# Kernel tuning notes

Hardware: AMD Instinct MI355X
Metric: run time of the kernel (lower is better)

Reference implementation:

```python
import jax, jax.numpy as jnp
import numpy as np

TEMPERATURE = 0.07


def setup_inputs() -> dict:
    key = jax.random.key(0)
    k1, k2 = jax.random.split(key)
    B, D = 8192, 256
    embeddings = jax.random.normal(k1, (B, D), dtype=jnp.float32)
    ids = jax.random.randint(k2, (B,), 0, 1024, dtype=jnp.int64 if jax.config.jax_enable_x64 else jnp.int32)
    return {"embeddings": embeddings, "ids": ids}


def reference(embeddings, ids):
    B = embeddings.shape[0]
    # L2-normalize rows (F.normalize with p=2, dim=1)
    emb = embeddings / jnp.maximum(jnp.linalg.norm(embeddings, axis=1, keepdims=True), 1e-12)
    sim = (emb @ emb.T) / TEMPERATURE                      # [B, B]
    eye = jnp.eye(B, dtype=bool)
    sim = jnp.where(eye, -jnp.inf, sim)
    exp_sim = jnp.exp(sim)                                  # diag -> 0
    pos_mask = (ids[:, None] == ids[None, :]) & ~eye        # [B, B]
    pos_sum = jnp.sum(jnp.where(pos_mask, exp_sim, 0.0), axis=1)  # [B]
    all_sum = jnp.sum(exp_sim, axis=1)                      # [B]
    valid = pos_mask.any(axis=1)
    per_row = -jnp.log(pos_sum / all_sum)
    loss = jnp.sum(jnp.where(valid, per_row, 0.0))
    n_valid = jnp.sum(valid.astype(jnp.float32))
    return loss / jnp.maximum(n_valid, 1.0)
```

## Files before the change

### kernel.cpp

```cpp
#include <hip/hip_runtime.h>
#include <hip/hip_bf16.h>

#define B_SZ 8192
#define D_SZ 256
#define NTILES 2080
#define GRID_SIM 512
#define PRESCALE 4.539816004686735f

typedef __attribute__((ext_vector_type(4))) float f32x4;
typedef __attribute__((ext_vector_type(8))) short s16x8;

__global__ __launch_bounds__(256) void norm_kernel(const float* __restrict__ emb,
                                                   ushort* __restrict__ nbf,
                                                   float* __restrict__ sums) {
    sums[blockIdx.x * 64 + (threadIdx.x >> 2)] = 0.0f;

    const int wave = threadIdx.x >> 6, lane = threadIdx.x & 63;
    for (int g = blockIdx.x; g < B_SZ / 4; g += 256) {
        const int row = g * 4 + wave;
        const float4 v = ((const float4*)(emb + (size_t)row * D_SZ))[lane];
        float ss = v.x * v.x + v.y * v.y + v.z * v.z + v.w * v.w;
        #pragma unroll
        for (int m = 1; m < 64; m <<= 1) ss += __shfl_xor(ss, m, 64);
        float s = PRESCALE / fmaxf(sqrtf(ss), 1e-12f);
        __hip_bfloat16 b0 = __float2bfloat16(v.x * s);
        __hip_bfloat16 b1 = __float2bfloat16(v.y * s);
        __hip_bfloat16 b2 = __float2bfloat16(v.z * s);
        __hip_bfloat16 b3 = __float2bfloat16(v.w * s);
        ushort4 o;
        o.x = *(ushort*)&b0; o.y = *(ushort*)&b1; o.z = *(ushort*)&b2; o.w = *(ushort*)&b3;
        ((ushort4*)(nbf + (size_t)row * D_SZ))[lane] = o;
    }
}

__device__ __forceinline__ void decode_tile(int tb, int& i0, int& j0, bool& diag) {
    int bj = (int)((sqrtf(8.0f * tb + 1.0f) - 1.0f) * 0.5f);
    while ((bj + 1) * (bj + 2) / 2 <= tb) ++bj;
    while (bj * (bj + 1) / 2 > tb) --bj;
    const int bi = tb - bj * (bj + 1) / 2;
    i0 = bi * 128; j0 = bj * 128; diag = (bi == bj);
}

__device__ __forceinline__ void gload16(const ushort* g, ushort* l) {
    __builtin_amdgcn_global_load_lds(
        (const __attribute__((address_space(1))) unsigned int*)g,
        (__attribute__((address_space(3))) unsigned int*)l,
        16, 0, 0);
}

__device__ __forceinline__ void issue_stage(ushort* bA,
                                            const ushort* __restrict__ N,
                                            int i0, int j0, int k0,
                                            int wave, int r, int c8s) {
    ushort* bB = bA + 8192;
    const ushort* gA = N + (size_t)(i0 + wave * 32) * D_SZ + k0;
    const ushort* gB = N + (size_t)(j0 + wave * 32) * D_SZ + k0;
    #pragma unroll
    for (int q = 0; q < 4; ++q) {
        gload16(gA + (size_t)(q * 8 + r) * D_SZ + c8s, bA + (wave * 32 + q * 8) * 64);
        gload16(gB + (size_t)(q * 8 + r) * D_SZ + c8s, bB + (wave * 32 + q * 8) * 64);
    }
}

__global__ __launch_bounds__(256) void sim_kernel(const ushort* __restrict__ N,
                                                  const int* __restrict__ ids,
                                                  float* __restrict__ all_sum,
                                                  float* __restrict__ pos_sum) {
    __shared__ ushort smem[4 * 128 * 64];

    const int t    = threadIdx.x;
    const int wave = t >> 6, lane = t & 63;
    const int wy   = wave >> 1, wx = wave & 1;
    const int r    = lane >> 3;
    const int c8s  = ((lane & 7) ^ r) * 8;
    const int hi   = lane >> 4, myc = lane & 15;

    int tb = blockIdx.x;
    int i0, j0; bool diag;
    decode_tile(tb, i0, j0, diag);

    issue_stage(smem, N, i0, j0, 0, wave, r, c8s);

    while (true) {
        const int ntb = tb + GRID_SIM;
        const bool have_next = (ntb < NTILES);
        int ni0 = i0, nj0 = j0; bool ndiag = diag;
        if (have_next) decode_tile(ntb, ni0, nj0, ndiag);

        f32x4 acc[4][4];
        #pragma unroll
        for (int mi = 0; mi < 4; ++mi)
            #pragma unroll
            for (int ni = 0; ni < 4; ++ni)
                acc[mi][ni] = (f32x4){0.f, 0.f, 0.f, 0.f};

        #pragma unroll
        for (int kk = 0; kk < 4; ++kk) {
            ushort* bA = smem + (kk & 1) * 16384;
            ushort* bW = smem + ((kk + 1) & 1) * 16384;
            ushort* bB = bA + 8192;

            asm volatile("s_waitcnt vmcnt(0)" ::: "memory");
            __syncthreads();
            if (kk < 3)           issue_stage(bW, N, i0, j0, (kk + 1) * 64, wave, r, c8s);
            else if (have_next)   issue_stage(bW, N, ni0, nj0, 0, wave, r, c8s);

            #pragma unroll
            for (int ks = 0; ks < 2; ++ks) {
                const int C = ks * 4 + (lane >> 4);
                const int slot = (C ^ (lane & 7)) * 8;
                s16x8 af[4], bf[4];
                #pragma unroll
                for (int mi = 0; mi < 4; ++mi)
                    af[mi] = *(const s16x8*)&bA[(wy * 64 + mi * 16 + (lane & 15)) * 64 + slot];
                #pragma unroll
                for (int ni = 0; ni < 4; ++ni)
                    bf[ni] = *(const s16x8*)&bB[(wx * 64 + ni * 16 + (lane & 15)) * 64 + slot];
                #pragma unroll
                for (int mi = 0; mi < 4; ++mi)
                    #pragma unroll
                    for (int ni = 0; ni < 4; ++ni)
                        acc[mi][ni] = __builtin_amdgcn_mfma_f32_16x16x32_bf16(
                            af[mi], bf[ni], acc[mi][ni], 0, 0, 0);
            }
        }

        int idc[4];
        #pragma unroll
        for (int ni = 0; ni < 4; ++ni)
            idc[ni] = ids[j0 + wx * 64 + ni * 16 + myc];

        float cAll[4] = {0.f, 0.f, 0.f, 0.f};
        float cPos[4] = {0.f, 0.f, 0.f, 0.f};

        #pragma unroll
        for (int mi = 0; mi < 4; ++mi) {
            float rAll[4] = {0.f, 0.f, 0.f, 0.f};
            float rPos[4] = {0.f, 0.f, 0.f, 0.f};
            const int rbase = wy * 64 + mi * 16 + hi * 4;
            const int4 idr  = *(const int4*)&ids[i0 + rbase];
            #pragma unroll
            for (int ni = 0; ni < 4; ++ni) {
                const int cloc = wx * 64 + ni * 16 + myc;
                #pragma unroll
                for (int rg = 0; rg < 4; ++rg) {
                    float e = __builtin_amdgcn_exp2f(acc[mi][ni][rg]);
                    if (diag && (rbase + rg) == cloc) e = 0.0f;
                    rAll[rg] += e; cAll[ni] += e;
                    const int idrv = (rg == 0) ? idr.x : (rg == 1) ? idr.y
                                   : (rg == 2) ? idr.z : idr.w;
                    if (idrv == idc[ni]) { rPos[rg] += e; cPos[ni] += e; }
                }
            }
            #pragma unroll
            for (int rg = 0; rg < 4; ++rg) {
                #pragma unroll
                for (int m = 1; m < 16; m <<= 1) {
                    rAll[rg] += __shfl_xor(rAll[rg], m, 64);
                    rPos[rg] += __shfl_xor(rPos[rg], m, 64);
                }
            }
            if (myc == 0) {
                #pragma unroll
                for (int rg = 0; rg < 4; ++rg) {
                    atomicAdd(&all_sum[i0 + rbase + rg], rAll[rg]);
                    if (rPos[rg] != 0.0f) atomicAdd(&pos_sum[i0 + rbase + rg], rPos[rg]);
                }
            }
        }

        if (!diag) {
            #pragma unroll
            for (int ni = 0; ni < 4; ++ni) {
                cAll[ni] += __shfl_xor(cAll[ni], 16, 64);
                cAll[ni] += __shfl_xor(cAll[ni], 32, 64);
                cPos[ni] += __shfl_xor(cPos[ni], 16, 64);
                cPos[ni] += __shfl_xor(cPos[ni], 32, 64);
            }
            if (lane < 16) {
                #pragma unroll
                for (int ni = 0; ni < 4; ++ni) {
                    const int gc = j0 + wx * 64 + ni * 16 + lane;
                    atomicAdd(&all_sum[gc], cAll[ni]);
                    if (cPos[ni] != 0.0f) atomicAdd(&pos_sum[gc], cPos[ni]);
                }
            }
        }

        if (!have_next) break;
        tb = ntb; i0 = ni0; j0 = nj0; diag = ndiag;
    }
}

__global__ __launch_bounds__(256) void loss_kernel(const float* __restrict__ all_sum,
                                                   const float* __restrict__ pos_sum,
                                                   float* __restrict__ out) {
    float loss = 0.0f, cnt = 0.0f;
    for (int i = threadIdx.x; i < B_SZ; i += 256) {
        float p = pos_sum[i], a = all_sum[i];
        if (p > 0.0f) { loss += logf(a) - logf(p); cnt += 1.0f; }
    }
    #pragma unroll
    for (int m = 1; m < 64; m <<= 1) {
        loss += __shfl_xor(loss, m, 64);
        cnt  += __shfl_xor(cnt, m, 64);
    }
    __shared__ float sl[4], sc[4];
    int wave = threadIdx.x >> 6, lane = threadIdx.x & 63;
    if (lane == 0) { sl[wave] = loss; sc[wave] = cnt; }
    __syncthreads();
    if (threadIdx.x == 0) {
        float L = sl[0] + sl[1] + sl[2] + sl[3];
        float C = sc[0] + sc[1] + sc[2] + sc[3];
        out[0] = L / fmaxf(C, 1.0f);
    }
}

extern "C" void kernel_launch(void* const* d_in, const int* in_sizes, int n_in,
                              void* d_out, int out_size, void* d_ws, size_t ws_size,
                              hipStream_t stream) {
    const float* emb = (const float*)d_in[0];
    const int*   ids = (const int*)d_in[1];
    float*       out = (float*)d_out;

    float*  all_sum = (float*)d_ws;
    float*  pos_sum = all_sum + B_SZ;
    ushort* nbf     = (ushort*)((char*)d_ws + 65536);

    norm_kernel<<<256, 256, 0, stream>>>(emb, nbf, all_sum);
    sim_kernel<<<GRID_SIM, 256, 0, stream>>>(nbf, ids, all_sum, pos_sum);
    loss_kernel<<<1, 256, 0, stream>>>(all_sum, pos_sum, out);
}
```

Measured before the change: 127.7 us.

## Load B operand directly from fragment-packed global layout and reduce rows via LDS

The norm kernel also writes a second copy of the normalized bf16 matrix, pre-packed in MFMA fragment order. The sim kernel now reads B fragments straight from global memory into registers instead of staging them through LDS, which halves the tile LDS footprint. Grid size goes up and occupancy is requested at 3 blocks per SM. Row partial sums now go through LDS and a block-wide reduction, giving one atomic per row per tile instead of shuffles plus per-wave atomics. In exchange it adds an extra global write in the norm pass, direct global loads on the MMA critical path with no prefetch, and an extra barrier per tile.

```diff
diff --git a/kernel.cpp b/kernel.cpp
--- a/kernel.cpp
+++ b/kernel.cpp
@@ -4,7 +4,7 @@
 #define B_SZ 8192
 #define D_SZ 256
 #define NTILES 2080
-#define GRID_SIM 512
+#define GRID_SIM 1040
 #define PRESCALE 4.539816004686735f
 
 typedef __attribute__((ext_vector_type(4))) float f32x4;
@@ -12,6 +12,7 @@
 
 __global__ __launch_bounds__(256) void norm_kernel(const float* __restrict__ emb,
                                                    ushort* __restrict__ nbf,
+                                                   ushort* __restrict__ nbf2,
                                                    float* __restrict__ sums) {
     sums[blockIdx.x * 64 + (threadIdx.x >> 2)] = 0.0f;
 
@@ -30,6 +31,10 @@
         ushort4 o;
         o.x = *(ushort*)&b0; o.y = *(ushort*)&b1; o.z = *(ushort*)&b2; o.w = *(ushort*)&b3;
         ((ushort4*)(nbf + (size_t)row * D_SZ))[lane] = o;
+        const int k0 = lane * 4;
+        const int f  = (row >> 4) * 8 + (k0 >> 5);
+        const int sl = (row & 15) + (((k0 >> 3) & 3) << 4);
+        *(ushort4*)(nbf2 + (size_t)f * 512 + sl * 8 + (k0 & 7)) = o;
     }
 }
 
@@ -48,25 +53,24 @@
         16, 0, 0);
 }
 
-__device__ __forceinline__ void issue_stage(ushort* bA,
-                                            const ushort* __restrict__ N,
-                                            int i0, int j0, int k0,
-                                            int wave, int r, int c8s) {
-    ushort* bB = bA + 8192;
+__device__ __forceinline__ void issue_stageA(ushort* bA,
+                                             const ushort* __restrict__ N,
+                                             int i0, int k0,
+                                             int wave, int r, int c8s) {
     const ushort* gA = N + (size_t)(i0 + wave * 32) * D_SZ + k0;
-    const ushort* gB = N + (size_t)(j0 + wave * 32) * D_SZ + k0;
     #pragma unroll
-    for (int q = 0; q < 4; ++q) {
+    for (int q = 0; q < 4; ++q)
         gload16(gA + (size_t)(q * 8 + r) * D_SZ + c8s, bA + (wave * 32 + q * 8) * 64);
-        gload16(gB + (size_t)(q * 8 + r) * D_SZ + c8s, bB + (wave * 32 + q * 8) * 64);
-    }
-}
-
-__global__ __launch_bounds__(256) void sim_kernel(const ushort* __restrict__ N,
-                                                  const int* __restrict__ ids,
-                                                  float* __restrict__ all_sum,
-                                                  float* __restrict__ pos_sum) {
-    __shared__ ushort smem[4 * 128 * 64];
+}
+
+__global__ __launch_bounds__(256, 3) void sim_kernel(const ushort* __restrict__ NA,
+                                                     const ushort* __restrict__ NB,
+                                                     const int* __restrict__ ids,
+                                                     float* __restrict__ all_sum,
+                                                     float* __restrict__ pos_sum) {
+    __shared__ ushort smem[2 * 128 * 64];
+    __shared__ float rowAllPart[16 * 129];
+    __shared__ float rowPosPart[16 * 129];
 
     const int t    = threadIdx.x;
     const int wave = t >> 6, lane = t & 63;
@@ -79,7 +83,7 @@
     int i0, j0; bool diag;
     decode_tile(tb, i0, j0, diag);
 
-    issue_stage(smem, N, i0, j0, 0, wave, r, c8s);
+    issue_stageA(smem, NA, i0, 0, wave, r, c8s);
 
     while (true) {
         const int ntb = tb + GRID_SIM;
@@ -94,28 +98,33 @@
             for (int ni = 0; ni < 4; ++ni)
                 acc[mi][ni] = (f32x4){0.f, 0.f, 0.f, 0.f};
 
+        const ushort* Bbase = NB + (size_t)((j0 >> 4) + wx * 4) * 8 * 512
+                                 + (size_t)lane * 8;
+
         #pragma unroll
         for (int kk = 0; kk < 4; ++kk) {
-            ushort* bA = smem + (kk & 1) * 16384;
-            ushort* bW = smem + ((kk + 1) & 1) * 16384;
-            ushort* bB = bA + 8192;
+            ushort* bA = smem + (kk & 1) * 8192;
+            ushort* bW = smem + ((kk + 1) & 1) * 8192;
 
             asm volatile("s_waitcnt vmcnt(0)" ::: "memory");
             __syncthreads();
-            if (kk < 3)           issue_stage(bW, N, i0, j0, (kk + 1) * 64, wave, r, c8s);
-            else if (have_next)   issue_stage(bW, N, ni0, nj0, 0, wave, r, c8s);
+            if (kk < 3)           issue_stageA(bW, NA, i0, (kk + 1) * 64, wave, r, c8s);
+            else if (have_next)   issue_stageA(bW, NA, ni0, 0, wave, r, c8s);
 
             #pragma unroll
             for (int ks = 0; ks < 2; ++ks) {
-                const int C = ks * 4 + (lane >> 4);
+                const int kc = kk * 2 + ks;
+                s16x8 bf[4];
+                #pragma unroll
+                for (int ni = 0; ni < 4; ++ni)
+                    bf[ni] = *(const s16x8*)(Bbase + (size_t)(ni * 8 + kc) * 512);
+
+                const int C = ks * 4 + hi;
                 const int slot = (C ^ (lane & 7)) * 8;
-                s16x8 af[4], bf[4];
+                s16x8 af[4];
                 #pragma unroll
                 for (int mi = 0; mi < 4; ++mi)
-                    af[mi] = *(const s16x8*)&bA[(wy * 64 + mi * 16 + (lane & 15)) * 64 + slot];
-                #pragma unroll
-                for (int ni = 0; ni < 4; ++ni)
-                    bf[ni] = *(const s16x8*)&bB[(wx * 64 + ni * 16 + (lane & 15)) * 64 + slot];
+                    af[mi] = *(const s16x8*)&bA[(wy * 64 + mi * 16 + myc) * 64 + slot];
                 #pragma unroll
                 for (int mi = 0; mi < 4; ++mi)
                     #pragma unroll
@@ -154,17 +163,15 @@
             }
             #pragma unroll
             for (int rg = 0; rg < 4; ++rg) {
-                #pragma unroll
-                for (int m = 1; m < 16; m <<= 1) {
-                    rAll[rg] += __shfl_xor(rAll[rg], m, 64);
-                    rPos[rg] += __shfl_xor(rPos[rg], m, 64);
-                }
-            }
-            if (myc == 0) {
+                rAll[rg] += __shfl_xor(rAll[rg], 1, 64);
+                rPos[rg] += __shfl_xor(rPos[rg], 1, 64);
+            }
+            if ((myc & 1) == 0) {
+                const int slot = wx * 8 + (myc >> 1);
                 #pragma unroll
                 for (int rg = 0; rg < 4; ++rg) {
-                    atomicAdd(&all_sum[i0 + rbase + rg], rAll[rg]);
-                    if (rPos[rg] != 0.0f) atomicAdd(&pos_sum[i0 + rbase + rg], rPos[rg]);
+                    rowAllPart[slot * 129 + rbase + rg] = rAll[rg];
+                    rowPosPart[slot * 129 + rbase + rg] = rPos[rg];
                 }
             }
         }
@@ -185,6 +192,17 @@
                     if (cPos[ni] != 0.0f) atomicAdd(&pos_sum[gc], cPos[ni]);
                 }
             }
+        }
+
+        __syncthreads();
+        {
+            const int row = t & 127;
+            const float* src = (t >= 128) ? rowPosPart : rowAllPart;
+            float s = 0.0f;
+            #pragma unroll
+            for (int sl = 0; sl < 16; ++sl) s += src[sl * 129 + row];
+            float* dst = (t >= 128) ? pos_sum : all_sum;
+            atomicAdd(&dst[i0 + row], s);
         }
 
         if (!have_next) break;
@@ -226,8 +244,9 @@
     float*  all_sum = (float*)d_ws;
     float*  pos_sum = all_sum + B_SZ;
     ushort* nbf     = (ushort*)((char*)d_ws + 65536);
-
-    norm_kernel<<<256, 256, 0, stream>>>(emb, nbf, all_sum);
-    sim_kernel<<<GRID_SIM, 256, 0, stream>>>(nbf, ids, all_sum, pos_sum);
+    ushort* nbf2    = nbf + (size_t)B_SZ * D_SZ;
+
+    norm_kernel<<<256, 256, 0, stream>>>(emb, nbf, nbf2, all_sum);
+    sim_kernel<<<GRID_SIM, 256, 0, stream>>>(nbf, nbf2, ids, all_sum, pos_sum);
     loss_kernel<<<1, 256, 0, stream>>>(all_sum, pos_sum, out);
 }
```

New measurement: 125.8 us. Within noise of the previous version (-1.5%).

## Use three-stage LDS ring with 32-wide K slices and LDS row-sum reduction

Applied to the files above, without the earlier changes.

Replaces the double-buffered 64-wide K staging with a three-slot ring of 32-wide K slices, using partial vmcnt waits and raw s_barrier so loads stay two stages ahead of the MFMA work. The swizzle and load mapping are changed to suit the narrower slices. Row partial sums are now written to padded LDS arrays and reduced by one thread per row before a single atomic each, replacing the shuffle trees and per-row atomics. The column-sum atomics now run unconditionally, adding zero on diagonal tiles, which adds atomic traffic. The hand-counted vmcnt values and barrier-only synchronization are fragile if the compiler's load counts differ.

```diff
diff --git a/kernel.cpp b/kernel.cpp
--- a/kernel.cpp
+++ b/kernel.cpp
@@ -6,6 +6,7 @@
 #define NTILES 2080
 #define GRID_SIM 512
 #define PRESCALE 4.539816004686735f
+#define RING_U 8192
 
 typedef __attribute__((ext_vector_type(4))) float f32x4;
 typedef __attribute__((ext_vector_type(8))) short s16x8;
@@ -48,17 +49,16 @@
         16, 0, 0);
 }
 
-__device__ __forceinline__ void issue_stage(ushort* bA,
+__device__ __forceinline__ void issue_stage(ushort* sl,
                                             const ushort* __restrict__ N,
                                             int i0, int j0, int k0,
-                                            int wave, int r, int c8s) {
-    ushort* bB = bA + 8192;
-    const ushort* gA = N + (size_t)(i0 + wave * 32) * D_SZ + k0;
-    const ushort* gB = N + (size_t)(j0 + wave * 32) * D_SZ + k0;
+                                            int wave, int srcoff) {
+    const ushort* gA = N + (size_t)(i0 + wave * 32) * D_SZ + k0 + srcoff;
+    const ushort* gB = N + (size_t)(j0 + wave * 32) * D_SZ + k0 + srcoff;
     #pragma unroll
-    for (int q = 0; q < 4; ++q) {
-        gload16(gA + (size_t)(q * 8 + r) * D_SZ + c8s, bA + (wave * 32 + q * 8) * 64);
-        gload16(gB + (size_t)(q * 8 + r) * D_SZ + c8s, bB + (wave * 32 + q * 8) * 64);
+    for (int q = 0; q < 2; ++q) {
+        gload16(gA + (size_t)(q * 16) * D_SZ, sl + (wave * 32 + q * 16) * 32);
+        gload16(gB + (size_t)(q * 16) * D_SZ, sl + 4096 + (wave * 32 + q * 16) * 32);
     }
 }
 
@@ -66,20 +66,26 @@
                                                   const int* __restrict__ ids,
                                                   float* __restrict__ all_sum,
                                                   float* __restrict__ pos_sum) {
-    __shared__ ushort smem[4 * 128 * 64];
+    __shared__ ushort smem[3 * RING_U];
+    __shared__ float pAll[128 * 17];
+    __shared__ float pPos[128 * 17];
 
     const int t    = threadIdx.x;
     const int wave = t >> 6, lane = t & 63;
     const int wy   = wave >> 1, wx = wave & 1;
-    const int r    = lane >> 3;
-    const int c8s  = ((lane & 7) ^ r) * 8;
     const int hi   = lane >> 4, myc = lane & 15;
+    const int srcoff = (lane >> 2) * D_SZ + (((lane & 3) ^ ((lane >> 2) & 3)) * 8);
+    const int slot8  = (hi ^ (myc & 3)) * 8;
 
     int tb = blockIdx.x;
     int i0, j0; bool diag;
     decode_tile(tb, i0, j0, diag);
 
-    issue_stage(smem, N, i0, j0, 0, wave, r, c8s);
+    issue_stage(smem,          N, i0, j0, 0,  wave, srcoff);
+    issue_stage(smem + RING_U, N, i0, j0, 32, wave, srcoff);
+    asm volatile("s_waitcnt vmcnt(0)" ::: "memory");
+
+    int rc = 0;
 
     while (true) {
         const int ntb = tb + GRID_SIM;
@@ -95,34 +101,36 @@
                 acc[mi][ni] = (f32x4){0.f, 0.f, 0.f, 0.f};
 
         #pragma unroll
-        for (int kk = 0; kk < 4; ++kk) {
-            ushort* bA = smem + (kk & 1) * 16384;
-            ushort* bW = smem + ((kk + 1) & 1) * 16384;
-            ushort* bB = bA + 8192;
-
-            asm volatile("s_waitcnt vmcnt(0)" ::: "memory");
-            __syncthreads();
-            if (kk < 3)           issue_stage(bW, N, i0, j0, (kk + 1) * 64, wave, r, c8s);
-            else if (have_next)   issue_stage(bW, N, ni0, nj0, 0, wave, r, c8s);
-
-            #pragma unroll
-            for (int ks = 0; ks < 2; ++ks) {
-                const int C = ks * 4 + (lane >> 4);
-                const int slot = (C ^ (lane & 7)) * 8;
-                s16x8 af[4], bf[4];
-                #pragma unroll
-                for (int mi = 0; mi < 4; ++mi)
-                    af[mi] = *(const s16x8*)&bA[(wy * 64 + mi * 16 + (lane & 15)) * 64 + slot];
+        for (int s = 0; s < 8; ++s) {
+            if (s < 2)       asm volatile("s_waitcnt vmcnt(13)" ::: "memory");
+            else if (s == 7) {
+                if (have_next) asm volatile("s_waitcnt vmcnt(4)" ::: "memory");
+                else           asm volatile("s_waitcnt vmcnt(0)" ::: "memory");
+            } else           asm volatile("s_waitcnt vmcnt(4)" ::: "memory");
+            __builtin_amdgcn_s_barrier();
+            __builtin_amdgcn_sched_barrier(0);
+
+            int ws = rc + 2; if (ws >= 3) ws -= 3;
+            if (s < 6)           issue_stage(smem + ws * RING_U, N, i0, j0, (s + 2) * 32, wave, srcoff);
+            else if (have_next)  issue_stage(smem + ws * RING_U, N, ni0, nj0, (s - 6) * 32, wave, srcoff);
+
+            const ushort* sA = smem + rc * RING_U;
+            const ushort* sB = sA + 4096;
+            s16x8 af[4], bf[4];
+            #pragma unroll
+            for (int mi = 0; mi < 4; ++mi)
+                af[mi] = *(const s16x8*)&sA[(wy * 64 + mi * 16 + myc) * 32 + slot8];
+            #pragma unroll
+            for (int ni = 0; ni < 4; ++ni)
+                bf[ni] = *(const s16x8*)&sB[(wx * 64 + ni * 16 + myc) * 32 + slot8];
+            #pragma unroll
+            for (int mi = 0; mi < 4; ++mi)
                 #pragma unroll
                 for (int ni = 0; ni < 4; ++ni)
-                    bf[ni] = *(const s16x8*)&bB[(wx * 64 + ni * 16 + (lane & 15)) * 64 + slot];
-                #pragma unroll
-                for (int mi = 0; mi < 4; ++mi)
-                    #pragma unroll
-                    for (int ni = 0; ni < 4; ++ni)
-                        acc[mi][ni] = __builtin_amdgcn_mfma_f32_16x16x32_bf16(
-                            af[mi], bf[ni], acc[mi][ni], 0, 0, 0);
-            }
+                    acc[mi][ni] = __builtin_amdgcn_mfma_f32_16x16x32_bf16(
+                        af[mi], bf[ni], acc[mi][ni], 0, 0, 0);
+
+            rc = rc + 1; if (rc >= 3) rc = 0;
         }
 
         int idc[4];
@@ -154,37 +162,47 @@
             }
             #pragma unroll
             for (int rg = 0; rg < 4; ++rg) {
-                #pragma unroll
-                for (int m = 1; m < 16; m <<= 1) {
-                    rAll[rg] += __shfl_xor(rAll[rg], m, 64);
-                    rPos[rg] += __shfl_xor(rPos[rg], m, 64);
-                }
-            }
-            if (myc == 0) {
+                rAll[rg] += __shfl_xor(rAll[rg], 1, 64);
+                rPos[rg] += __shfl_xor(rPos[rg], 1, 64);
+            }
+            if ((myc & 1) == 0) {
+                const int slot = wx * 8 + (myc >> 1);
                 #pragma unroll
                 for (int rg = 0; rg < 4; ++rg) {
-                    atomicAdd(&all_sum[i0 + rbase + rg], rAll[rg]);
-                    if (rPos[rg] != 0.0f) atomicAdd(&pos_sum[i0 + rbase + rg], rPos[rg]);
+                    pAll[(rbase + rg) * 17 + slot] = rAll[rg];
+                    pPos[(rbase + rg) * 17 + slot] = rPos[rg];
                 }
             }
         }
 
-        if (!diag) {
+        #pragma unroll
+        for (int ni = 0; ni < 4; ++ni) {
+            cAll[ni] += __shfl_xor(cAll[ni], 16, 64);
+            cAll[ni] += __shfl_xor(cAll[ni], 32, 64);
+            cPos[ni] += __shfl_xor(cPos[ni], 16, 64);
+            cPos[ni] += __shfl_xor(cPos[ni], 32, 64);
+        }
+        if (lane < 16) {
             #pragma unroll
             for (int ni = 0; ni < 4; ++ni) {
-                cAll[ni] += __shfl_xor(cAll[ni], 16, 64);
-                cAll[ni] += __shfl_xor(cAll[ni], 32, 64);
-                cPos[ni] += __shfl_xor(cPos[ni], 16, 64);
-                cPos[ni] += __shfl_xor(cPos[ni], 32, 64);
-            }
-            if (lane < 16) {
-                #pragma unroll
-                for (int ni = 0; ni < 4; ++ni) {
-                    const int gc = j0 + wx * 64 + ni * 16 + lane;
-                    atomicAdd(&all_sum[gc], cAll[ni]);
-                    if (cPos[ni] != 0.0f) atomicAdd(&pos_sum[gc], cPos[ni]);
-                }
-            }
+                const int gc = j0 + wx * 64 + ni * 16 + lane;
+                atomicAdd(&all_sum[gc], diag ? 0.0f : cAll[ni]);
+                atomicAdd(&pos_sum[gc], diag ? 0.0f : cPos[ni]);
+            }
+        }
+
+        asm volatile("s_waitcnt lgkmcnt(0)" ::: "memory");
+        __builtin_amdgcn_s_barrier();
+        __builtin_amdgcn_sched_barrier(0);
+
+        {
+            const int row = t & 127;
+            const float* src = (t >= 128) ? pPos : pAll;
+            float s = 0.0f;
+            #pragma unroll
+            for (int sl = 0; sl < 16; ++sl) s += src[row * 17 + sl];
+            float* dst = (t >= 128) ? pos_sum : all_sum;
+            atomicAdd(&dst[i0 + row], s);
         }
 
         if (!have_next) break;
```

After: 127.7 us. No clear change (+0.0%).

## Replace global atomics with per-slot partial sums and a parallel reduce kernel

Applied to the files above, without the earlier changes.

Row and column sums from each similarity tile are no longer atomically added into two global arrays. Each tile now writes its partials into a dedicated slot of a 130-slot buffer. A 32-block reduce kernel sums the slots per row, computes the per-row loss, and atomically accumulates two scalars, and a final one-thread kernel divides them. The sim grid grows from 512 to 1040 blocks. This removes atomic contention and replaces the single-block loss kernel, but adds about 8.5 MB of partial-buffer traffic and an extra launch.

```diff
diff --git a/kernel.cpp b/kernel.cpp
--- a/kernel.cpp
+++ b/kernel.cpp
@@ -4,7 +4,9 @@
 #define B_SZ 8192
 #define D_SZ 256
 #define NTILES 2080
-#define GRID_SIM 512
+#define GRID_SIM 1040
+#define SL 8192
+#define NSLOT 130
 #define PRESCALE 4.539816004686735f
 
 typedef __attribute__((ext_vector_type(4))) float f32x4;
@@ -12,8 +14,8 @@
 
 __global__ __launch_bounds__(256) void norm_kernel(const float* __restrict__ emb,
                                                    ushort* __restrict__ nbf,
-                                                   float* __restrict__ sums) {
-    sums[blockIdx.x * 64 + (threadIdx.x >> 2)] = 0.0f;
+                                                   float* __restrict__ acc2) {
+    if (blockIdx.x == 0 && threadIdx.x < 2) acc2[threadIdx.x] = 0.0f;
 
     const int wave = threadIdx.x >> 6, lane = threadIdx.x & 63;
     for (int g = blockIdx.x; g < B_SZ / 4; g += 256) {
@@ -64,8 +66,8 @@
 
 __global__ __launch_bounds__(256) void sim_kernel(const ushort* __restrict__ N,
                                                   const int* __restrict__ ids,
-                                                  float* __restrict__ all_sum,
-                                                  float* __restrict__ pos_sum) {
+                                                  float* __restrict__ allP,
+                                                  float* __restrict__ posP) {
     __shared__ ushort smem[4 * 128 * 64];
 
     const int t    = threadIdx.x;
@@ -107,15 +109,15 @@
 
             #pragma unroll
             for (int ks = 0; ks < 2; ++ks) {
-                const int C = ks * 4 + (lane >> 4);
+                const int C = ks * 4 + hi;
                 const int slot = (C ^ (lane & 7)) * 8;
                 s16x8 af[4], bf[4];
                 #pragma unroll
                 for (int mi = 0; mi < 4; ++mi)
-                    af[mi] = *(const s16x8*)&bA[(wy * 64 + mi * 16 + (lane & 15)) * 64 + slot];
+                    af[mi] = *(const s16x8*)&bA[(wy * 64 + mi * 16 + myc) * 64 + slot];
                 #pragma unroll
                 for (int ni = 0; ni < 4; ++ni)
-                    bf[ni] = *(const s16x8*)&bB[(wx * 64 + ni * 16 + (lane & 15)) * 64 + slot];
+                    bf[ni] = *(const s16x8*)&bB[(wx * 64 + ni * 16 + myc) * 64 + slot];
                 #pragma unroll
                 for (int mi = 0; mi < 4; ++mi)
                     #pragma unroll
@@ -124,6 +126,10 @@
                             af[mi], bf[ni], acc[mi][ni], 0, 0, 0);
             }
         }
+
+        const int bi = i0 >> 7, bj = j0 >> 7;
+        const int slotR = 2 * (bj - bi) + wx;
+        const int slotC = 129 - 2 * bi - wy;
 
         int idc[4];
         #pragma unroll
@@ -161,29 +167,26 @@
                 }
             }
             if (myc == 0) {
-                #pragma unroll
-                for (int rg = 0; rg < 4; ++rg) {
-                    atomicAdd(&all_sum[i0 + rbase + rg], rAll[rg]);
-                    if (rPos[rg] != 0.0f) atomicAdd(&pos_sum[i0 + rbase + rg], rPos[rg]);
-                }
-            }
-        }
-
-        if (!diag) {
+                float4 sa = {rAll[0], rAll[1], rAll[2], rAll[3]};
+                float4 sp = {rPos[0], rPos[1], rPos[2], rPos[3]};
+                *(float4*)&allP[(size_t)slotR * SL + i0 + rbase] = sa;
+                *(float4*)&posP[(size_t)slotR * SL + i0 + rbase] = sp;
+            }
+        }
+
+        #pragma unroll
+        for (int ni = 0; ni < 4; ++ni) {
+            cAll[ni] += __shfl_xor(cAll[ni], 16, 64);
+            cAll[ni] += __shfl_xor(cAll[ni], 32, 64);
+            cPos[ni] += __shfl_xor(cPos[ni], 16, 64);
+            cPos[ni] += __shfl_xor(cPos[ni], 32, 64);
+        }
+        if (lane < 16) {
             #pragma unroll
             for (int ni = 0; ni < 4; ++ni) {
-                cAll[ni] += __shfl_xor(cAll[ni], 16, 64);
-                cAll[ni] += __shfl_xor(cAll[ni], 32, 64);
-                cPos[ni] += __shfl_xor(cPos[ni], 16, 64);
-                cPos[ni] += __shfl_xor(cPos[ni], 32, 64);
-            }
-            if (lane < 16) {
-                #pragma unroll
-                for (int ni = 0; ni < 4; ++ni) {
-                    const int gc = j0 + wx * 64 + ni * 16 + lane;
-                    atomicAdd(&all_sum[gc], cAll[ni]);
-                    if (cPos[ni] != 0.0f) atomicAdd(&pos_sum[gc], cPos[ni]);
-                }
+                const int gc = j0 + wx * 64 + ni * 16 + lane;
+                allP[(size_t)slotC * SL + gc] = diag ? 0.0f : cAll[ni];
+                posP[(size_t)slotC * SL + gc] = diag ? 0.0f : cPos[ni];
             }
         }
 
@@ -192,28 +195,34 @@
     }
 }
 
-__global__ __launch_bounds__(256) void loss_kernel(const float* __restrict__ all_sum,
-                                                   const float* __restrict__ pos_sum,
-                                                   float* __restrict__ out) {
+__global__ __launch_bounds__(256) void reduce_kernel(const float* __restrict__ allP,
+                                                     const float* __restrict__ posP,
+                                                     float* __restrict__ acc2) {
+    const int row = blockIdx.x * 256 + threadIdx.x;
+    float a = 0.0f, p = 0.0f;
+    for (int s = 0; s < NSLOT; ++s) {
+        a += allP[(size_t)s * SL + row];
+        p += posP[(size_t)s * SL + row];
+    }
     float loss = 0.0f, cnt = 0.0f;
-    for (int i = threadIdx.x; i < B_SZ; i += 256) {
-        float p = pos_sum[i], a = all_sum[i];
-        if (p > 0.0f) { loss += logf(a) - logf(p); cnt += 1.0f; }
-    }
+    if (p > 0.0f) { loss = logf(a) - logf(p); cnt = 1.0f; }
     #pragma unroll
     for (int m = 1; m < 64; m <<= 1) {
         loss += __shfl_xor(loss, m, 64);
         cnt  += __shfl_xor(cnt, m, 64);
     }
     __shared__ float sl[4], sc[4];
-    int wave = threadIdx.x >> 6, lane = threadIdx.x & 63;
+    const int wave = threadIdx.x >> 6, lane = threadIdx.x & 63;
     if (lane == 0) { sl[wave] = loss; sc[wave] = cnt; }
     __syncthreads();
     if (threadIdx.x == 0) {
-        float L = sl[0] + sl[1] + sl[2] + sl[3];
-        float C = sc[0] + sc[1] + sc[2] + sc[3];
-        out[0] = L / fmaxf(C, 1.0f);
-    }
+        atomicAdd(&acc2[0], sl[0] + sl[1] + sl[2] + sl[3]);
+        atomicAdd(&acc2[1], sc[0] + sc[1] + sc[2] + sc[3]);
+    }
+}
+
+__global__ void final_kernel(const float* __restrict__ acc2, float* __restrict__ out) {
+    out[0] = acc2[0] / fmaxf(acc2[1], 1.0f);
 }
 
 extern "C" void kernel_launch(void* const* d_in, const int* in_sizes, int n_in,
@@ -223,11 +232,13 @@
     const int*   ids = (const int*)d_in[1];
     float*       out = (float*)d_out;
 
-    float*  all_sum = (float*)d_ws;
-    float*  pos_sum = all_sum + B_SZ;
-    ushort* nbf     = (ushort*)((char*)d_ws + 65536);
-
-    norm_kernel<<<256, 256, 0, stream>>>(emb, nbf, all_sum);
-    sim_kernel<<<GRID_SIM, 256, 0, stream>>>(nbf, ids, all_sum, pos_sum);
-    loss_kernel<<<1, 256, 0, stream>>>(all_sum, pos_sum, out);
-}
+    float*  acc2 = (float*)d_ws;
+    float*  allP = (float*)((char*)d_ws + 4096);
+    float*  posP = allP + (size_t)NSLOT * SL;
+    ushort* nbf  = (ushort*)(posP + (size_t)NSLOT * SL);
+
+    norm_kernel<<<256, 256, 0, stream>>>(emb, nbf, acc2);
+    sim_kernel<<<GRID_SIM, 256, 0, stream>>>(nbf, ids, allP, posP);
+    reduce_kernel<<<32, 256, 0, stream>>>(allP, posP, acc2);
+    final_kernel<<<1, 1, 0, stream>>>(acc2, out);
+}
```

Measured after the change: 129.1 us. About the same (+1.1%).
